# Optimization experiments

Hardware: AMD Instinct MI355X
Metric: run time of the kernel (lower is better)

## Reference

```python
import jax, jax.numpy as jnp
import numpy as np

V, D, DI, S, B, NI = 32000, 1024, 768, 512, 8, 197
EPS = 1e-5

def _ln(x, g, b):
    m = jnp.mean(x, axis=-1, keepdims=True)
    v = jnp.var(x, axis=-1, keepdims=True)
    return (x - m) * jax.lax.rsqrt(v + EPS) * g + b

def _pos_enc(seq_len, d):
    pos = np.arange(seq_len)[:, None].astype(np.float32)
    i = np.arange(0, d, 2).astype(np.float32)
    ang = pos / np.power(10000.0, i / d)
    pe = np.zeros((seq_len, d), dtype=np.float32)
    pe[:, 0::2] = np.sin(ang)
    pe[:, 1::2] = np.cos(ang)
    return jnp.asarray(pe)

def setup_inputs() -> dict:
    key = jax.random.key(0)
    ks = jax.random.split(key, 24)
    def rn(k, shape, scale=0.02):
        return jax.random.normal(k, shape, dtype=jnp.float32) * scale
    return {
        'tokens': jax.random.randint(ks[0], (B, S), 0, V),
        'img_emb': jax.random.normal(ks[1], (B, NI, DI), dtype=jnp.float32),
        'emb_table': rn(ks[2], (V, D), 1.0),
        'Wq1': rn(ks[3], (D, D)), 'bq1': jnp.zeros((D,), jnp.float32),
        'Wk1': rn(ks[4], (D, D)), 'bk1': jnp.zeros((D,), jnp.float32),
        'Wv1': rn(ks[5], (D, D)), 'bv1': jnp.zeros((D,), jnp.float32),
        'g1': jnp.ones((D,), jnp.float32), 'b1': jnp.zeros((D,), jnp.float32),
        'Wq2': rn(ks[6], (D, D)), 'bq2': jnp.zeros((D,), jnp.float32),
        'Wk2': rn(ks[7], (DI, D)), 'bk2': jnp.zeros((D,), jnp.float32),
        'Wv2': rn(ks[8], (DI, D)), 'bv2': jnp.zeros((D,), jnp.float32),
        'g2': jnp.ones((D,), jnp.float32), 'b2': jnp.zeros((D,), jnp.float32),
        'Wp': rn(ks[9], (D, V)), 'bp': jnp.zeros((V,), jnp.float32),
    }

def _forward(tokens, img_emb, emb_table, Wq1, bq1, Wk1, bk1, Wv1, bv1, g1, b1,
             Wq2, bq2, Wk2, bk2, Wv2, bv2, g2, b2, Wp, bp):
    scale = 1.0 / jnp.sqrt(jnp.float32(D))
    x = emb_table[tokens] + _pos_enc(S, D)[None]  # [B,S,D]
    # masked (causal) self-attention
    Q = x @ Wq1 + bq1
    K = x @ Wk1 + bk1
    Vv = x @ Wv1 + bv1
    attn = jnp.einsum('bqd,bkd->bqk', Q, K) * scale
    causal = jnp.tril(jnp.ones((S, S), dtype=bool))
    attn = jnp.where(causal[None], attn, -jnp.inf)
    A = jax.nn.softmax(attn, axis=-1)
    x = _ln(A @ Vv + x, g1, b1)
    # cross-attention over image tokens
    Q2 = x @ Wq2 + bq2
    K2 = img_emb @ Wk2 + bk2
    V2 = img_emb @ Wv2 + bv2
    A2 = jax.nn.softmax(jnp.einsum('bqd,bkd->bqk', Q2, K2) * scale, axis=-1)
    x = _ln(A2 @ V2 + x, g2, b2)
    # vocab projection (note: Decoder.forward never calls self.ff)
    return x @ Wp + bp  # [B,S,V]

def reference(tokens, img_emb, emb_table, Wq1, bq1, Wk1, bk1, Wv1, bv1, g1, b1,
              Wq2, bq2, Wk2, bk2, Wv2, bv2, g2, b2, Wp, bp):
    return _forward(tokens, img_emb, emb_table, Wq1, bq1, Wk1, bk1, Wv1, bv1, g1, b1,
                    Wq2, bq2, Wk2, bk2, Wv2, bv2, g2, b2, Wp, bp)
```

## Files before the change

### kernel.cpp

```cpp
#include <hip/hip_runtime.h>
#include <hip/hip_bf16.h>


#define DEV __device__ __forceinline__

typedef __bf16 bf16x8 __attribute__((ext_vector_type(8)));
typedef float f32x4 __attribute__((ext_vector_type(4)));
typedef unsigned int u32;
typedef __hip_bfloat16 bf16;

DEV void llds16(const void* g, void* l) {
  __builtin_amdgcn_global_load_lds((const __attribute__((address_space(1))) u32*)g,
                                   (__attribute__((address_space(3))) u32*)l, 16, 0, 0);
}

DEV float wredsum(float v){
#pragma unroll
  for (int o = 32; o; o >>= 1) v += __shfl_xor(v, o, 64);
  return v;
}
DEV float wredmax(float v){
#pragma unroll
  for (int o = 32; o; o >>= 1) v = fmaxf(v, __shfl_xor(v, o, 64));
  return v;
}

DEV float b2f(unsigned short x){ return __uint_as_float((u32)x << 16); }

DEV void store_out(float* p, float v){ *p = v; }
DEV void store_out(bf16* p, float v){ *p = __float2bfloat16(v); }

#define SBAR __builtin_amdgcn_sched_barrier(0)
#define HBAR __builtin_amdgcn_s_barrier()
#define LGKM0 asm volatile("s_waitcnt lgkmcnt(0)" ::: "memory")
#define VMC6 asm volatile("s_waitcnt vmcnt(6)" ::: "memory")
#define VMC0 asm volatile("s_waitcnt vmcnt(0)" ::: "memory")

#define RD_A(slot, mh) do { \
  _Pragma("unroll") for (int m = 0; m < 4; m++) { \
    const int r_ = wr*128 + ((mh)*4 + m)*16 + lo; \
    _Pragma("unroll") for (int ks = 0; ks < 2; ks++) \
      af[m*2+ks] = *(const bf16x8*)((slot) + r_*128 + ((((ks<<2)|hi) ^ x7) << 4)); \
  } } while(0)
#define RD_B(slot, nh) do { \
  _Pragma("unroll") for (int n = 0; n < 2; n++) { \
    const int gn_ = (nh)*2 + n; \
    const int r_ = wc*64 + gn_*16 + lo; \
    _Pragma("unroll") for (int ks = 0; ks < 2; ks++) \
      bfv[gn_*2+ks] = *(const bf16x8*)((slot) + 32768 + r_*128 + ((((ks<<2)|hi) ^ x7) << 4)); \
  } } while(0)
#define MQ(mh, nh) do { \
  __builtin_amdgcn_s_setprio(1); \
  _Pragma("unroll") for (int ks = 0; ks < 2; ks++) \
  _Pragma("unroll") for (int m = 0; m < 4; m++) \
  _Pragma("unroll") for (int n = 0; n < 2; n++) \
    acc[(mh)*4+m][(nh)*2+n] = __builtin_amdgcn_mfma_f32_16x16x32_bf16( \
        af[m*2+ks], bfv[((nh)*2+n)*2+ks], acc[(mh)*4+m][(nh)*2+n], 0, 0, 0); \
  __builtin_amdgcn_s_setprio(0); \
  } while(0)

template<typename OutT>
__global__ __launch_bounds__(512, 1) void gemm256_kernel(
    const bf16* __restrict__ A, const bf16* __restrict__ Bt, OutT* __restrict__ C,
    const float* __restrict__ bias, int M, int N, int K, int lda, int ldb, int ldc)
{
  __shared__ alignas(16) char lds[131072];
  const int tid = threadIdx.x;
  const int wave = tid >> 6, lane = tid & 63;
  const int lo = lane & 15, hi = lane >> 4;
  const int x7 = lo & 7;
  const int wr = wave >> 2, wc = wave & 3;
  const int lr8 = lane >> 3;
  const int koff = ((lane & 7) ^ lr8) << 3;

  const int nbx = M >> 8;
  const int nwg = nbx * (N >> 8);
  int id = blockIdx.x;
  int g = (nwg & 7) ? id : ((id & 7) * (nwg >> 3) + (id >> 3));
  const int row0 = (g % nbx) * 256, col0 = (g / nbx) * 256;
  const int NT2 = K >> 6;

  auto stage = [&](int kind, int t) {
    if (t >= NT2) return;
    char* slot = lds + (t & 1) * 65536;
    const int kk = (t << 6) + koff;
#pragma unroll
    for (int j = 0; j < 2; j++) {
      if (kind == 0 || kind == 3) {
        const int br = ((kind == 3) ? 64 : 0) + j*128 + wave*8;
        llds16(A + (long)(row0 + br + lr8)*lda + kk, slot + br*128);
      } else {
        const int br = ((kind == 2) ? 32 : 0) + (wave&3)*8 + (wave>>2)*64 + j*128;
        llds16(Bt + (long)(col0 + br + lr8)*ldb + kk, slot + 32768 + br*128);
      }
    }
  };

  f32x4 acc[8][4] = {};
  bf16x8 af[8], bfv[8];

  stage(0,0); stage(1,0); stage(2,0); stage(3,0);
  stage(0,1); stage(1,1); stage(2,1);
  VMC6;
  HBAR; SBAR;

  for (int it = 0; it < (NT2 >> 1); it++) {
    const int ta = it*2, tb = ta+1;
    const char* sa = lds;
    const char* sb = lds + 65536;
    RD_A(sa, 0); RD_B(sa, 0); SBAR; stage(3, tb); SBAR;
    HBAR; LGKM0; SBAR; MQ(0, 0); SBAR; HBAR; SBAR;
    RD_B(sa, 1); SBAR; stage(0, ta+2); SBAR;
    HBAR; LGKM0; SBAR; MQ(0, 1); SBAR; HBAR; SBAR;
    RD_A(sa, 1); SBAR; stage(1, ta+2); SBAR;
    HBAR; LGKM0; SBAR; MQ(1, 0); SBAR; HBAR; SBAR;
    stage(2, ta+2); SBAR;
    HBAR; SBAR; MQ(1, 1); SBAR;
    if (ta+2 < NT2) { VMC6; } else { VMC0; }
    HBAR; SBAR;
    RD_A(sb, 0); RD_B(sb, 0); SBAR; stage(3, ta+2); SBAR;
    HBAR; LGKM0; SBAR; MQ(0, 0); SBAR; HBAR; SBAR;
    RD_B(sb, 1); SBAR; stage(0, tb+2); SBAR;
    HBAR; LGKM0; SBAR; MQ(0, 1); SBAR; HBAR; SBAR;
    RD_A(sb, 1); SBAR; stage(1, tb+2); SBAR;
    HBAR; LGKM0; SBAR; MQ(1, 0); SBAR; HBAR; SBAR;
    stage(2, tb+2); SBAR;
    HBAR; SBAR; MQ(1, 1); SBAR;
    if (tb+2 < NT2) { VMC6; } else { VMC0; }
    HBAR; SBAR;
  }

#pragma unroll
  for (int m = 0; m < 8; m++) {
    const int r = row0 + wr * 128 + m * 16 + hi * 4;
#pragma unroll
    for (int n = 0; n < 4; n++) {
      const int c = col0 + wc * 64 + n * 16 + lo;
      const float bb = bias ? bias[c] : 0.0f;
#pragma unroll
      for (int j = 0; j < 4; j++)
        store_out(&C[(long)(r + j) * ldc + c], acc[m][n][j] + bb);
    }
  }
}

template<typename OutT>
__global__ __launch_bounds__(256) void gemm_bt_kernel(
    const bf16* __restrict__ A, const bf16* __restrict__ Bt, OutT* __restrict__ C,
    const float* __restrict__ bias, int M, int N, int K,
    int lda, int ldb, int ldc, long sA, long sB, long sC, int tri, int kcausal)
{
  A  += (long)blockIdx.z * sA;
  Bt += (long)blockIdx.z * sB;
  C  += (long)blockIdx.z * sC;
  __shared__ alignas(16) char lds[32768];
  int bx = blockIdx.x, by = blockIdx.y;
  if (tri) { int t = blockIdx.x, i = 0; while (t > i) { t -= i + 1; i++; } bx = i; by = t; }
  const int tid = threadIdx.x;
  const int wave = tid >> 6, lane = tid & 63;
  const int lo = lane & 15, hi = lane >> 4;
  const int hi2 = hi ^ ((lo >> 1) & 3);
  const int wr = wave >> 1, wc = wave & 1;
  const int row0 = bx * 128, col0 = by * 128;
  const int srow  = lane >> 2;
  const int skoff = (((lane & 3) ^ ((lane >> 3) & 3)) << 3);
  const int Keff = kcausal ? (K < row0 + 128 ? K : row0 + 128) : K;
  const int NT = Keff >> 5;

  auto stage = [&](int t) {
    char* base = lds + (t & 1) * 16384;
    const int kk = (t << 5) + skoff;
#pragma unroll
    for (int c = 0; c < 2; ++c) {
      const int seg = c*4 + wave;
      int ra = row0 + seg*16 + srow; ra = ra < M ? ra : M-1;
      llds16(A + (long)ra*lda + kk, base + seg*1024);
      int rb = col0 + seg*16 + srow; rb = rb < N ? rb : N-1;
      llds16(Bt + (long)rb*ldb + kk, base + 8192 + seg*1024);
    }
  };

  f32x4 acc[4][4] = {};

  stage(0);
  VMC0;
  HBAR; SBAR;

  for (int t = 0; t < NT; t++) {
    const char* As = lds + (t & 1) * 16384;
    const char* Bs = As + 8192;
    if (t + 1 < NT) stage(t + 1);
    bf16x8 af[4], bfv[4];
#pragma unroll
    for (int m = 0; m < 4; m++)
      af[m] = *(const bf16x8*)(As + ((wr*64 + m*16 + lo) << 6) + (hi2 << 4));
#pragma unroll
    for (int n = 0; n < 4; n++)
      bfv[n] = *(const bf16x8*)(Bs + ((wc*64 + n*16 + lo) << 6) + (hi2 << 4));
    __builtin_amdgcn_s_setprio(1);
#pragma unroll
    for (int m = 0; m < 4; m++)
#pragma unroll
      for (int n = 0; n < 4; n++)
        acc[m][n] = __builtin_amdgcn_mfma_f32_16x16x32_bf16(af[m], bfv[n], acc[m][n], 0, 0, 0);
    __builtin_amdgcn_s_setprio(0);
    SBAR;
    VMC0;
    SBAR;
    HBAR; SBAR;
  }

#pragma unroll
  for (int m = 0; m < 4; m++) {
    const int rbase = row0 + wr*64 + m*16 + hi*4;
#pragma unroll
    for (int n = 0; n < 4; n++) {
      const int cc = col0 + wc*64 + n*16 + lo;
      if (cc >= N) continue;
      const float bb = bias ? bias[cc] : 0.0f;
#pragma unroll
      for (int j = 0; j < 4; j++) {
        const int rr = rbase + j;
        if (rr < M) store_out(&C[(long)rr*ldc + cc], acc[m][n][j] + bb);
      }
    }
  }
}

__global__ __launch_bounds__(256) void wprep4_kernel(
    const float* W0, const float* W1, const float* W2, const float* W3,
    bf16* T0, bf16* T1, bf16* T2, bf16* T3, int K, int N)
{
  const int z = blockIdx.z;
  const float* W = z == 0 ? W0 : z == 1 ? W1 : z == 2 ? W2 : W3;
  bf16* T = z == 0 ? T0 : z == 1 ? T1 : z == 2 ? T2 : T3;
  __shared__ bf16 t[32][33];
  const int k0 = blockIdx.x * 32, n0 = blockIdx.y * 32;
  const int tx = threadIdx.x & 31, ty = threadIdx.x >> 5;
#pragma unroll
  for (int i = 0; i < 4; i++)
    t[ty + i*8][tx] = __float2bfloat16(W[(long)(k0 + ty + i*8)*N + n0 + tx]);
  __syncthreads();
#pragma unroll
  for (int i = 0; i < 4; i++)
    T[(long)(n0 + ty + i*8)*K + k0 + tx] = t[tx][ty + i*8];
}

__global__ __launch_bounds__(256) void transpose_pad_kernel(
    const bf16* __restrict__ in, bf16* __restrict__ out,
    int R, int Cc, int inLD, int outLD, long inBatch, long outBatch)
{
  in  += (long)blockIdx.z * inBatch;
  out += (long)blockIdx.z * outBatch;
  __shared__ bf16 t[32][33];
  const int r0 = blockIdx.x * 32, c0 = blockIdx.y * 32;
  const int tx = threadIdx.x & 31, ty = threadIdx.x >> 5;
#pragma unroll
  for (int i = 0; i < 4; i++) {
    const int r = r0 + ty + i*8;
    bf16 v = __float2bfloat16(0.0f);
    if (r < R) v = in[(long)r*inLD + c0 + tx];
    t[ty + i*8][tx] = v;
  }
  __syncthreads();
#pragma unroll
  for (int i = 0; i < 4; i++) {
    const int oc = r0 + tx;
    const int orow = c0 + ty + i*8;
    if (oc < outLD) out[(long)orow*outLD + oc] = t[tx][ty + i*8];
  }
}

__global__ __launch_bounds__(256) void concat_bias_kernel(
    const float* a, const float* b, const float* c, int n1, int n2, int n3, float* out)
{
  const int i = blockIdx.x * 256 + threadIdx.x;
  if (i >= n1 + n2 + n3) return;
  out[i] = i < n1 ? a[i] : (i < n1 + n2 ? b[i - n1] : c[i - n1 - n2]);
}

__global__ __launch_bounds__(256) void embed_kernel(
    const int* __restrict__ tok, const float* __restrict__ tbl,
    bf16* __restrict__ xb)
{
  const int row = blockIdx.x;
  const int s = row & 511;
  const float pos = (float)s;
  const float* te = tbl + (long)tok[row] * 1024;
  const int d0 = threadIdx.x * 4;
  float4 v = *(const float4*)(te + d0);
  float o[4] = {v.x, v.y, v.z, v.w};
#pragma unroll
  for (int k = 0; k < 4; k++) {
    const int d = d0 + k;
    const int i2 = d & ~1;
    const float ang = pos * exp2f((float)i2 * -0.0129762816f);
    o[k] += (d & 1) ? __cosf(ang) : __sinf(ang);
  }
  bf16 ob[4];
#pragma unroll
  for (int k = 0; k < 4; k++) ob[k] = __float2bfloat16(o[k]);
  *(ushort4*)((unsigned short*)xb + (long)row*1024 + d0) = *(ushort4*)ob;
}

__global__ __launch_bounds__(256) void cvt_bf16_kernel(const float* __restrict__ in, bf16* __restrict__ out, long n)
{
  long i = (long)blockIdx.x * blockDim.x + threadIdx.x;
  if (i < n) out[i] = __float2bfloat16(in[i]);
}

__global__ __launch_bounds__(64) void softmax_causal_kernel(
    const float* __restrict__ Sc, bf16* __restrict__ P)
{
  const int row = blockIdx.x;
  const int q = row & 511;
  const float* srow = Sc + (long)row * 512;
  bf16* prow = P + (long)row * 512;
  const int lane = threadIdx.x;
  const float scale = 0.03125f;
  float mx = -1e30f;
  for (int j = lane; j <= q; j += 64) mx = fmaxf(mx, srow[j]);
  mx = wredmax(mx);
  float sum = 0.0f;
  for (int j = lane; j <= q; j += 64) sum += expf((srow[j] - mx) * scale);
  sum = wredsum(sum);
  const float inv = 1.0f / sum;
  for (int j = lane; j < 512; j += 64) {
    float p = (j <= q) ? expf((srow[j] - mx) * scale) * inv : 0.0f;
    prow[j] = __float2bfloat16(p);
  }
}

__global__ __launch_bounds__(64) void softmax_cross_kernel(
    const float* __restrict__ Sc, bf16* __restrict__ P)
{
  const int row = blockIdx.x;
  const float* srow = Sc + (long)row * 224;
  bf16* prow = P + (long)row * 224;
  const int lane = threadIdx.x;
  const float scale = 0.03125f;
  float mx = -1e30f;
  for (int j = lane; j < 197; j += 64) mx = fmaxf(mx, srow[j]);
  mx = wredmax(mx);
  float sum = 0.0f;
  for (int j = lane; j < 197; j += 64) sum += expf((srow[j] - mx) * scale);
  sum = wredsum(sum);
  const float inv = 1.0f / sum;
  for (int j = lane; j < 224; j += 64) {
    float p = (j < 197) ? expf((srow[j] - mx) * scale) * inv : 0.0f;
    prow[j] = __float2bfloat16(p);
  }
}

__global__ __launch_bounds__(256) void add_ln_kernel(
    const bf16* __restrict__ Acc, const bf16* __restrict__ Res,
    const float* __restrict__ g, const float* __restrict__ b,
    bf16* __restrict__ outb)
{
  const int row = blockIdx.x;
  const unsigned short* a = (const unsigned short*)Acc + (long)row * 1024;
  const unsigned short* r = (const unsigned short*)Res + (long)row * 1024;
  const int d0 = threadIdx.x * 4;
  ushort4 av = *(const ushort4*)(a + d0);
  ushort4 rv = *(const ushort4*)(r + d0);
  float vals[4] = { b2f(av.x) + b2f(rv.x), b2f(av.y) + b2f(rv.y),
                    b2f(av.z) + b2f(rv.z), b2f(av.w) + b2f(rv.w) };
  float s = vals[0] + vals[1] + vals[2] + vals[3];
  float ss = vals[0]*vals[0] + vals[1]*vals[1] + vals[2]*vals[2] + vals[3]*vals[3];
  s = wredsum(s); ss = wredsum(ss);
  __shared__ float sh[8];
  const int wave = threadIdx.x >> 6, lane = threadIdx.x & 63;
  if (lane == 0) { sh[wave] = s; sh[wave+4] = ss; }
  __syncthreads();
  s  = sh[0] + sh[1] + sh[2] + sh[3];
  ss = sh[4] + sh[5] + sh[6] + sh[7];
  const float mean = s * (1.0f/1024.0f);
  const float var  = ss * (1.0f/1024.0f) - mean*mean;
  const float inv  = rsqrtf(var + 1e-5f);
  bf16 ob[4];
#pragma unroll
  for (int i = 0; i < 4; i++) {
    const int d = d0 + i;
    ob[i] = __float2bfloat16((vals[i] - mean) * inv * g[d] + b[d]);
  }
  *(ushort4*)((unsigned short*)outb + (long)row*1024 + d0) = *(ushort4*)ob;
}

extern "C" void kernel_launch(void* const* d_in, const int* in_sizes, int n_in,
                              void* d_out, int out_size, void* d_ws, size_t ws_size,
                              hipStream_t stream) {
  const int*   tokens = (const int*)  d_in[0];
  const float* img    = (const float*)d_in[1];
  const float* emb    = (const float*)d_in[2];
  const float* Wq1    = (const float*)d_in[3];
  const float* bq1    = (const float*)d_in[4];
  const float* Wk1    = (const float*)d_in[5];
  const float* bk1    = (const float*)d_in[6];
  const float* Wv1    = (const float*)d_in[7];
  const float* bv1    = (const float*)d_in[8];
  const float* g1     = (const float*)d_in[9];
  const float* b1     = (const float*)d_in[10];
  const float* Wq2    = (const float*)d_in[11];
  const float* bq2    = (const float*)d_in[12];
  const float* Wk2    = (const float*)d_in[13];
  const float* bk2    = (const float*)d_in[14];
  const float* Wv2    = (const float*)d_in[15];
  const float* bv2    = (const float*)d_in[16];
  const float* g2     = (const float*)d_in[17];
  const float* b2     = (const float*)d_in[18];
  const float* Wp     = (const float*)d_in[19];
  const float* bp     = (const float*)d_in[20];
  float* out = (float*)d_out;

  const int B = 8, S = 512, D = 1024, DI = 768, NI = 197, NIP = 224, V = 32000;
  const int M = B * S;
  const int MI = B * NI;

  char* ws = (char*)d_ws;
  size_t off = 0;
  auto alloc = [&](size_t bytes) -> char* {
    char* p = ws + off; off += (bytes + 255) & ~(size_t)255; return p;
  };
  bf16* Wq1t = (bf16*)alloc((size_t)D*D*2);
  bf16* Wk1t = (bf16*)alloc((size_t)D*D*2);
  bf16* Wv1t = (bf16*)alloc((size_t)D*D*2);
  bf16* Wq2t = (bf16*)alloc((size_t)D*D*2);
  bf16* Wk2t = (bf16*)alloc((size_t)D*DI*2);
  bf16* Wv2t = (bf16*)alloc((size_t)D*DI*2);
  bf16* Wpt  = (bf16*)alloc((size_t)V*D*2);
  float* bqkv= (float*)alloc((size_t)3*D*4);
  float* bkv2= (float*)alloc((size_t)2*D*4);
  bf16*  xb  = (bf16*) alloc((size_t)M*D*2);
  bf16*  imgb= (bf16*) alloc((size_t)MI*DI*2);
  bf16*  QKV = (bf16*) alloc((size_t)M*3*D*2);
  bf16*  Vt  = (bf16*) alloc((size_t)M*D*2);
  float* sc1 = (float*)alloc((size_t)B*S*S*4);
  bf16*  P1  = (bf16*) alloc((size_t)B*S*S*2);
  bf16*  ao1 = (bf16*) alloc((size_t)M*D*2);
  bf16*  x2b = (bf16*) alloc((size_t)M*D*2);
  bf16*  Q2  = (bf16*) alloc((size_t)M*D*2);
  bf16*  KV2 = (bf16*) alloc((size_t)MI*2*D*2);
  bf16*  V2t = (bf16*) alloc((size_t)B*D*NIP*2);
  float* sc2 = (float*)alloc((size_t)B*S*NIP*4);
  bf16*  P2  = (bf16*) alloc((size_t)B*S*NIP*2);
  bf16*  ao2 = (bf16*) alloc((size_t)M*D*2);
  bf16*  x3b = (bf16*) alloc((size_t)M*D*2);
  (void)ws_size; (void)in_sizes; (void)n_in; (void)out_size;

  wprep4_kernel<<<dim3(D/32,  D/32, 4), 256, 0, stream>>>(Wq1, Wk1, Wv1, Wq2, Wq1t, Wk1t, Wv1t, Wq2t, D, D);
  wprep4_kernel<<<dim3(DI/32, D/32, 2), 256, 0, stream>>>(Wk2, Wv2, nullptr, nullptr, Wk2t, Wv2t, nullptr, nullptr, DI, D);
  wprep4_kernel<<<dim3(D/32,  V/32, 1), 256, 0, stream>>>(Wp, nullptr, nullptr, nullptr, Wpt, nullptr, nullptr, nullptr, D, V);
  concat_bias_kernel<<<(3*D+255)/256, 256, 0, stream>>>(bq1, bk1, bv1, D, D, D, bqkv);
  concat_bias_kernel<<<(2*D+255)/256, 256, 0, stream>>>(bk2, bv2, nullptr, D, D, 0, bkv2);

  embed_kernel<<<M, 256, 0, stream>>>(tokens, emb, xb);
  {
    long n = (long)MI * DI;
    cvt_bf16_kernel<<<(int)((n + 255)/256), 256, 0, stream>>>(img, imgb, n);
  }

  auto gemmF = [&](const bf16* A, const bf16* Bt, float* C, const float* bias,
                   int m, int n, int k, int lda, int ldb, int ldc,
                   long sA, long sB, long sC, int batch) {
    dim3 g((m+127)/128, (n+127)/128, batch);
    gemm_bt_kernel<float><<<g, 256, 0, stream>>>(A, Bt, C, bias, m, n, k, lda, ldb, ldc, sA, sB, sC, 0, 0);
  };
  auto gemmB = [&](const bf16* A, const bf16* Bt, bf16* C, const float* bias,
                   int m, int n, int k, int lda, int ldb, int ldc,
                   long sA, long sB, long sC, int batch) {
    dim3 g((m+127)/128, (n+127)/128, batch);
    gemm_bt_kernel<bf16><<<g, 256, 0, stream>>>(A, Bt, C, bias, m, n, k, lda, ldb, ldc, sA, sB, sC, 0, 0);
  };

  gemm256_kernel<bf16><<<dim3((M/256)*(3*D/256)), 512, 0, stream>>>(
      xb, Wq1t, QKV, bqkv, M, 3*D, D, D, D, 3*D);
  transpose_pad_kernel<<<dim3(S/32, D/32, B), 256, 0, stream>>>(
      QKV + 2*D, Vt, S, D, 3*D, S, (long)S*3*D, (long)D*S);
  gemm_bt_kernel<float><<<dim3(10, 1, B), 256, 0, stream>>>(
      QKV, QKV + D, sc1, nullptr, S, S, D, 3*D, 3*D, S,
      (long)S*3*D, (long)S*3*D, (long)S*S, 1, 0);
  softmax_causal_kernel<<<M, 64, 0, stream>>>(sc1, P1);
  gemm_bt_kernel<bf16><<<dim3(S/128, D/128, B), 256, 0, stream>>>(
      P1, Vt, ao1, nullptr, S, D, S, S, S, D,
      (long)S*S, (long)D*S, (long)S*D, 0, 1);
  add_ln_kernel<<<M, 256, 0, stream>>>(ao1, xb, g1, b1, x2b);

  gemm256_kernel<bf16><<<dim3((M/256)*(D/256)), 512, 0, stream>>>(
      x2b, Wq2t, Q2, bq2, M, D, D, D, D, D);
  gemmB(imgb, Wk2t, KV2, bkv2, MI, 2*D, DI, DI, DI, 2*D, 0, 0, 0, 1);
  transpose_pad_kernel<<<dim3((NIP+31)/32, D/32, B), 256, 0, stream>>>(
      KV2 + D, V2t, NI, D, 2*D, NIP, (long)NI*2*D, (long)D*NIP);
  gemmF(Q2, KV2, sc2, nullptr, S, NI, D, D, 2*D, NIP, (long)S*D, (long)NI*2*D, (long)S*NIP, B);
  softmax_cross_kernel<<<M, 64, 0, stream>>>(sc2, P2);
  gemmB(P2, V2t, ao2, nullptr, S, D, NIP, NIP, NIP, D, (long)S*NIP, (long)D*NIP, (long)S*D, B);
  add_ln_kernel<<<M, 256, 0, stream>>>(ao2, x2b, g2, b2, x3b);

  gemm256_kernel<float><<<dim3((M/256)*(V/256)), 512, 0, stream>>>(
      x3b, Wpt, out, bp, M, V, D, D, D, V);
}
```

Measured before the change: 636.0 us.

## Produce transposed V directly via swapped-operand GEMMs and drop transpose kernels

The V projections for self- and cross-attention are now computed as W^T·X GEMMs, so they write V already transposed. This removes the two separate transpose_pad kernels and the extra traffic through the QKV and KV2 buffers. The V bias is moved into the P·V GEMM epilogue, which is valid because each softmax row sums to one. Image tokens are padded to 224 per batch during the bf16 conversion so that the cross-attention GEMMs work on aligned tiles. The cost is that the fused QKV GEMM becomes a QK GEMM plus a separate V GEMM on the smaller 128-tile kernel. Padded rows of V2t now contain Wv2·0 rather than zero, which relies on softmax masking those columns and on the bias being added per column.

```diff
diff --git a/kernel.cpp b/kernel.cpp
--- a/kernel.cpp
+++ b/kernel.cpp
@@ -246,31 +246,6 @@
     T[(long)(n0 + ty + i*8)*K + k0 + tx] = t[tx][ty + i*8];
 }
 
-__global__ __launch_bounds__(256) void transpose_pad_kernel(
-    const bf16* __restrict__ in, bf16* __restrict__ out,
-    int R, int Cc, int inLD, int outLD, long inBatch, long outBatch)
-{
-  in  += (long)blockIdx.z * inBatch;
-  out += (long)blockIdx.z * outBatch;
-  __shared__ bf16 t[32][33];
-  const int r0 = blockIdx.x * 32, c0 = blockIdx.y * 32;
-  const int tx = threadIdx.x & 31, ty = threadIdx.x >> 5;
-#pragma unroll
-  for (int i = 0; i < 4; i++) {
-    const int r = r0 + ty + i*8;
-    bf16 v = __float2bfloat16(0.0f);
-    if (r < R) v = in[(long)r*inLD + c0 + tx];
-    t[ty + i*8][tx] = v;
-  }
-  __syncthreads();
-#pragma unroll
-  for (int i = 0; i < 4; i++) {
-    const int oc = r0 + tx;
-    const int orow = c0 + ty + i*8;
-    if (oc < outLD) out[(long)orow*outLD + oc] = t[tx][ty + i*8];
-  }
-}
-
 __global__ __launch_bounds__(256) void concat_bias_kernel(
     const float* a, const float* b, const float* c, int n1, int n2, int n3, float* out)
 {
@@ -303,10 +278,16 @@
   *(ushort4*)((unsigned short*)xb + (long)row*1024 + d0) = *(ushort4*)ob;
 }
 
-__global__ __launch_bounds__(256) void cvt_bf16_kernel(const float* __restrict__ in, bf16* __restrict__ out, long n)
-{
-  long i = (long)blockIdx.x * blockDim.x + threadIdx.x;
-  if (i < n) out[i] = __float2bfloat16(in[i]);
+__global__ __launch_bounds__(256) void cvt_pad_img_kernel(
+    const float* __restrict__ img, bf16* __restrict__ imgb)
+{
+  const long i = (long)blockIdx.x * 256 + threadIdx.x;
+  if (i >= (long)1792 * 768) return;
+  const int pr = (int)(i / 768), col = (int)(i % 768);
+  const int b = pr / 224, tok = pr % 224;
+  float v = 0.0f;
+  if (tok < 197) v = img[((long)b * 197 + tok) * 768 + col];
+  imgb[i] = __float2bfloat16(v);
 }
 
 __global__ __launch_bounds__(64) void softmax_causal_kernel(
@@ -414,7 +395,7 @@
 
   const int B = 8, S = 512, D = 1024, DI = 768, NI = 197, NIP = 224, V = 32000;
   const int M = B * S;
-  const int MI = B * NI;
+  const int MIP = B * NIP;
 
   char* ws = (char*)d_ws;
   size_t off = 0;
@@ -428,19 +409,18 @@
   bf16* Wk2t = (bf16*)alloc((size_t)D*DI*2);
   bf16* Wv2t = (bf16*)alloc((size_t)D*DI*2);
   bf16* Wpt  = (bf16*)alloc((size_t)V*D*2);
-  float* bqkv= (float*)alloc((size_t)3*D*4);
-  float* bkv2= (float*)alloc((size_t)2*D*4);
+  float* bqk = (float*)alloc((size_t)2*D*4);
   bf16*  xb  = (bf16*) alloc((size_t)M*D*2);
-  bf16*  imgb= (bf16*) alloc((size_t)MI*DI*2);
-  bf16*  QKV = (bf16*) alloc((size_t)M*3*D*2);
-  bf16*  Vt  = (bf16*) alloc((size_t)M*D*2);
+  bf16*  imgb= (bf16*) alloc((size_t)MIP*DI*2);
+  bf16*  QK  = (bf16*) alloc((size_t)M*2*D*2);
+  bf16*  Vt  = (bf16*) alloc((size_t)D*M*2);
   float* sc1 = (float*)alloc((size_t)B*S*S*4);
   bf16*  P1  = (bf16*) alloc((size_t)B*S*S*2);
   bf16*  ao1 = (bf16*) alloc((size_t)M*D*2);
   bf16*  x2b = (bf16*) alloc((size_t)M*D*2);
   bf16*  Q2  = (bf16*) alloc((size_t)M*D*2);
-  bf16*  KV2 = (bf16*) alloc((size_t)MI*2*D*2);
-  bf16*  V2t = (bf16*) alloc((size_t)B*D*NIP*2);
+  bf16*  K2p = (bf16*) alloc((size_t)MIP*D*2);
+  bf16*  V2t = (bf16*) alloc((size_t)D*MIP*2);
   float* sc2 = (float*)alloc((size_t)B*S*NIP*4);
   bf16*  P2  = (bf16*) alloc((size_t)B*S*NIP*2);
   bf16*  ao2 = (bf16*) alloc((size_t)M*D*2);
@@ -450,49 +430,40 @@
   wprep4_kernel<<<dim3(D/32,  D/32, 4), 256, 0, stream>>>(Wq1, Wk1, Wv1, Wq2, Wq1t, Wk1t, Wv1t, Wq2t, D, D);
   wprep4_kernel<<<dim3(DI/32, D/32, 2), 256, 0, stream>>>(Wk2, Wv2, nullptr, nullptr, Wk2t, Wv2t, nullptr, nullptr, DI, D);
   wprep4_kernel<<<dim3(D/32,  V/32, 1), 256, 0, stream>>>(Wp, nullptr, nullptr, nullptr, Wpt, nullptr, nullptr, nullptr, D, V);
-  concat_bias_kernel<<<(3*D+255)/256, 256, 0, stream>>>(bq1, bk1, bv1, D, D, D, bqkv);
-  concat_bias_kernel<<<(2*D+255)/256, 256, 0, stream>>>(bk2, bv2, nullptr, D, D, 0, bkv2);
+  concat_bias_kernel<<<(2*D+255)/256, 256, 0, stream>>>(bq1, bk1, nullptr, D, D, 0, bqk);
 
   embed_kernel<<<M, 256, 0, stream>>>(tokens, emb, xb);
   {
-    long n = (long)MI * DI;
-    cvt_bf16_kernel<<<(int)((n + 255)/256), 256, 0, stream>>>(img, imgb, n);
-  }
-
-  auto gemmF = [&](const bf16* A, const bf16* Bt, float* C, const float* bias,
-                   int m, int n, int k, int lda, int ldb, int ldc,
-                   long sA, long sB, long sC, int batch) {
-    dim3 g((m+127)/128, (n+127)/128, batch);
-    gemm_bt_kernel<float><<<g, 256, 0, stream>>>(A, Bt, C, bias, m, n, k, lda, ldb, ldc, sA, sB, sC, 0, 0);
-  };
-  auto gemmB = [&](const bf16* A, const bf16* Bt, bf16* C, const float* bias,
-                   int m, int n, int k, int lda, int ldb, int ldc,
-                   long sA, long sB, long sC, int batch) {
-    dim3 g((m+127)/128, (n+127)/128, batch);
-    gemm_bt_kernel<bf16><<<g, 256, 0, stream>>>(A, Bt, C, bias, m, n, k, lda, ldb, ldc, sA, sB, sC, 0, 0);
-  };
-
-  gemm256_kernel<bf16><<<dim3((M/256)*(3*D/256)), 512, 0, stream>>>(
-      xb, Wq1t, QKV, bqkv, M, 3*D, D, D, D, 3*D);
-  transpose_pad_kernel<<<dim3(S/32, D/32, B), 256, 0, stream>>>(
-      QKV + 2*D, Vt, S, D, 3*D, S, (long)S*3*D, (long)D*S);
+    long n = (long)MIP * DI;
+    cvt_pad_img_kernel<<<(int)((n + 255)/256), 256, 0, stream>>>(img, imgb);
+  }
+
+  gemm256_kernel<bf16><<<dim3((M/256)*(2*D/256)), 512, 0, stream>>>(
+      xb, Wq1t, QK, bqk, M, 2*D, D, D, D, 2*D);
+  gemm_bt_kernel<bf16><<<dim3(D/128, M/128, 1), 256, 0, stream>>>(
+      Wv1t, xb, Vt, nullptr, D, M, D, D, D, M, 0, 0, 0, 0, 0);
   gemm_bt_kernel<float><<<dim3(10, 1, B), 256, 0, stream>>>(
-      QKV, QKV + D, sc1, nullptr, S, S, D, 3*D, 3*D, S,
-      (long)S*3*D, (long)S*3*D, (long)S*S, 1, 0);
+      QK, QK + D, sc1, nullptr, S, S, D, 2*D, 2*D, S,
+      (long)S*2*D, (long)S*2*D, (long)S*S, 1, 0);
   softmax_causal_kernel<<<M, 64, 0, stream>>>(sc1, P1);
   gemm_bt_kernel<bf16><<<dim3(S/128, D/128, B), 256, 0, stream>>>(
-      P1, Vt, ao1, nullptr, S, D, S, S, S, D,
-      (long)S*S, (long)D*S, (long)S*D, 0, 1);
+      P1, Vt, ao1, bv1, S, D, S, S, M, D,
+      (long)S*S, (long)S, (long)S*D, 0, 1);
   add_ln_kernel<<<M, 256, 0, stream>>>(ao1, xb, g1, b1, x2b);
 
   gemm256_kernel<bf16><<<dim3((M/256)*(D/256)), 512, 0, stream>>>(
       x2b, Wq2t, Q2, bq2, M, D, D, D, D, D);
-  gemmB(imgb, Wk2t, KV2, bkv2, MI, 2*D, DI, DI, DI, 2*D, 0, 0, 0, 1);
-  transpose_pad_kernel<<<dim3((NIP+31)/32, D/32, B), 256, 0, stream>>>(
-      KV2 + D, V2t, NI, D, 2*D, NIP, (long)NI*2*D, (long)D*NIP);
-  gemmF(Q2, KV2, sc2, nullptr, S, NI, D, D, 2*D, NIP, (long)S*D, (long)NI*2*D, (long)S*NIP, B);
+  gemm_bt_kernel<bf16><<<dim3(MIP/128, D/128, 1), 256, 0, stream>>>(
+      imgb, Wk2t, K2p, bk2, MIP, D, DI, DI, DI, D, 0, 0, 0, 0, 0);
+  gemm_bt_kernel<bf16><<<dim3(D/128, MIP/128, 1), 256, 0, stream>>>(
+      Wv2t, imgb, V2t, nullptr, D, MIP, DI, DI, DI, MIP, 0, 0, 0, 0, 0);
+  gemm_bt_kernel<float><<<dim3(S/128, (NIP+127)/128, B), 256, 0, stream>>>(
+      Q2, K2p, sc2, nullptr, S, NI, D, D, D, NIP,
+      (long)S*D, (long)NIP*D, (long)S*NIP, 0, 0);
   softmax_cross_kernel<<<M, 64, 0, stream>>>(sc2, P2);
-  gemmB(P2, V2t, ao2, nullptr, S, D, NIP, NIP, NIP, D, (long)S*NIP, (long)D*NIP, (long)S*D, B);
+  gemm_bt_kernel<bf16><<<dim3(S/128, D/128, B), 256, 0, stream>>>(
+      P2, V2t, ao2, bv2, S, D, NIP, NIP, MIP, D,
+      (long)S*NIP, (long)NIP, (long)S*D, 0, 0);
   add_ln_kernel<<<M, 256, 0, stream>>>(ao2, x2b, g2, b2, x3b);
 
   gemm256_kernel<float><<<dim3((M/256)*(V/256)), 512, 0, stream>>>(
```

Result: slower. 679.4 us (+6.8%).

## Fuse softmax into the P@V GEMM for self and cross attention

Applied to the files above, without the earlier changes.

Removes the standalone causal and cross softmax kernels and the bf16 probability buffers. A new fused_pv_kernel computes per-row max and sum from the fp32 score matrix in a prologue, then builds normalized bf16 probability tiles directly in LDS while streaming V through global_load_lds. This drops a kernel launch and a round trip of the probability matrix per attention, but each block recomputes exponentials from global scores with scalar loads, so the A-operand path depends on uncoalesced fp32 reads and redundant exp work across column blocks.

```diff
diff --git a/kernel.cpp b/kernel.cpp
--- a/kernel.cpp
+++ b/kernel.cpp
@@ -17,11 +17,6 @@
 DEV float wredsum(float v){
 #pragma unroll
   for (int o = 32; o; o >>= 1) v += __shfl_xor(v, o, 64);
-  return v;
-}
-DEV float wredmax(float v){
-#pragma unroll
-  for (int o = 32; o; o >>= 1) v = fmaxf(v, __shfl_xor(v, o, 64));
   return v;
 }
 
@@ -148,7 +143,7 @@
 __global__ __launch_bounds__(256) void gemm_bt_kernel(
     const bf16* __restrict__ A, const bf16* __restrict__ Bt, OutT* __restrict__ C,
     const float* __restrict__ bias, int M, int N, int K,
-    int lda, int ldb, int ldc, long sA, long sB, long sC, int tri, int kcausal)
+    int lda, int ldb, int ldc, long sA, long sB, long sC, int tri)
 {
   A  += (long)blockIdx.z * sA;
   Bt += (long)blockIdx.z * sB;
@@ -164,8 +159,7 @@
   const int row0 = bx * 128, col0 = by * 128;
   const int srow  = lane >> 2;
   const int skoff = (((lane & 3) ^ ((lane >> 3) & 3)) << 3);
-  const int Keff = kcausal ? (K < row0 + 128 ? K : row0 + 128) : K;
-  const int NT = Keff >> 5;
+  const int NT = K >> 5;
 
   auto stage = [&](int t) {
     char* base = lds + (t & 1) * 16384;
@@ -227,6 +221,111 @@
   }
 }
 
+template<int CAUSAL>
+__global__ __launch_bounds__(256) void fused_pv_kernel(
+    const float* __restrict__ Sc, const bf16* __restrict__ Bt, bf16* __restrict__ C,
+    int Kw, int validFixed, int ldS, int ldb, int ldc, long sS, long sB, long sC)
+{
+  Sc += (long)blockIdx.z * sS;
+  Bt += (long)blockIdx.z * sB;
+  C  += (long)blockIdx.z * sC;
+  __shared__ alignas(16) char lds[32768];
+  __shared__ float smx[128], sinv[128];
+  const int tid = threadIdx.x;
+  const int wave = tid >> 6, lane = tid & 63;
+  const int lo = lane & 15, hi = lane >> 4;
+  const int hi2 = hi ^ ((lo >> 1) & 3);
+  const int wr = wave >> 1, wc = wave & 1;
+  const int row0 = blockIdx.x * 128, col0 = blockIdx.y * 128;
+  const int srow  = lane >> 2;
+  const int skoff = (((lane & 3) ^ ((lane >> 3) & 3)) << 3);
+  const int Keff = CAUSAL ? (Kw < row0 + 128 ? Kw : row0 + 128) : Kw;
+  const int NT = Keff >> 5;
+  const float scale = 0.03125f;
+
+  {
+    const int r2 = tid >> 1, par = tid & 1;
+    const float* sr = Sc + (long)(row0 + r2) * ldS;
+    const int valid = CAUSAL ? (row0 + r2 + 1) : validFixed;
+    float mx = -3.0e38f;
+    for (int j = par; j < valid; j += 2) mx = fmaxf(mx, sr[j]);
+    mx = fmaxf(mx, __shfl_xor(mx, 1, 64));
+    float sum = 0.0f;
+    for (int j = par; j < valid; j += 2) sum += expf((sr[j] - mx) * scale);
+    sum += __shfl_xor(sum, 1, 64);
+    if (par == 0) { smx[r2] = mx; sinv[r2] = 1.0f / sum; }
+  }
+  __syncthreads();
+
+  auto writeA = [&](int t) {
+    char* base = lds + (t & 1) * 16384;
+    const int r2 = tid >> 1, par = tid & 1;
+    const float* sr = Sc + (long)(row0 + r2) * ldS;
+    const int valid = CAUSAL ? (row0 + r2 + 1) : validFixed;
+    const float mx = smx[r2], inv = sinv[r2];
+#pragma unroll
+    for (int i = 0; i < 2; i++) {
+      const int gq = par * 2 + i;
+      const int k0 = (t << 5) + gq * 8;
+      bf16 p8[8];
+#pragma unroll
+      for (int jj = 0; jj < 8; jj++) {
+        const int k = k0 + jj;
+        float p = (k < valid) ? expf((sr[k] - mx) * scale) * inv : 0.0f;
+        p8[jj] = __float2bfloat16(p);
+      }
+      *(bf16x8*)(base + (r2 << 6) + ((gq ^ ((r2 >> 1) & 3)) << 4)) = *(bf16x8*)p8;
+    }
+  };
+  auto stageB = [&](int t) {
+    char* base = lds + (t & 1) * 16384 + 8192;
+    const int kk = (t << 5) + skoff;
+#pragma unroll
+    for (int c = 0; c < 2; ++c) {
+      const int seg = c*4 + wave;
+      llds16(Bt + (long)(col0 + seg*16 + srow)*ldb + kk, base + seg*1024);
+    }
+  };
+
+  f32x4 acc[4][4] = {};
+
+  writeA(0); stageB(0);
+  __syncthreads();
+
+  for (int t = 0; t < NT; t++) {
+    const char* As = lds + (t & 1) * 16384;
+    const char* Bs = As + 8192;
+    if (t + 1 < NT) { stageB(t + 1); writeA(t + 1); }
+    bf16x8 af[4], bfv[4];
+#pragma unroll
+    for (int m = 0; m < 4; m++)
+      af[m] = *(const bf16x8*)(As + ((wr*64 + m*16 + lo) << 6) + (hi2 << 4));
+#pragma unroll
+    for (int n = 0; n < 4; n++)
+      bfv[n] = *(const bf16x8*)(Bs + ((wc*64 + n*16 + lo) << 6) + (hi2 << 4));
+    __builtin_amdgcn_s_setprio(1);
+#pragma unroll
+    for (int m = 0; m < 4; m++)
+#pragma unroll
+      for (int n = 0; n < 4; n++)
+        acc[m][n] = __builtin_amdgcn_mfma_f32_16x16x32_bf16(af[m], bfv[n], acc[m][n], 0, 0, 0);
+    __builtin_amdgcn_s_setprio(0);
+    __syncthreads();
+  }
+
+#pragma unroll
+  for (int m = 0; m < 4; m++) {
+    const int rbase = row0 + wr*64 + m*16 + hi*4;
+#pragma unroll
+    for (int n = 0; n < 4; n++) {
+      const int cc = col0 + wc*64 + n*16 + lo;
+#pragma unroll
+      for (int j = 0; j < 4; j++)
+        C[(long)(rbase + j)*ldc + cc] = __float2bfloat16(acc[m][n][j]);
+    }
+  }
+}
+
 __global__ __launch_bounds__(256) void wprep4_kernel(
     const float* W0, const float* W1, const float* W2, const float* W3,
     bf16* T0, bf16* T1, bf16* T2, bf16* T3, int K, int N)
@@ -307,49 +406,6 @@
 {
   long i = (long)blockIdx.x * blockDim.x + threadIdx.x;
   if (i < n) out[i] = __float2bfloat16(in[i]);
-}
-
-__global__ __launch_bounds__(64) void softmax_causal_kernel(
-    const float* __restrict__ Sc, bf16* __restrict__ P)
-{
-  const int row = blockIdx.x;
-  const int q = row & 511;
-  const float* srow = Sc + (long)row * 512;
-  bf16* prow = P + (long)row * 512;
-  const int lane = threadIdx.x;
-  const float scale = 0.03125f;
-  float mx = -1e30f;
-  for (int j = lane; j <= q; j += 64) mx = fmaxf(mx, srow[j]);
-  mx = wredmax(mx);
-  float sum = 0.0f;
-  for (int j = lane; j <= q; j += 64) sum += expf((srow[j] - mx) * scale);
-  sum = wredsum(sum);
-  const float inv = 1.0f / sum;
-  for (int j = lane; j < 512; j += 64) {
-    float p = (j <= q) ? expf((srow[j] - mx) * scale) * inv : 0.0f;
-    prow[j] = __float2bfloat16(p);
-  }
-}
-
-__global__ __launch_bounds__(64) void softmax_cross_kernel(
-    const float* __restrict__ Sc, bf16* __restrict__ P)
-{
-  const int row = blockIdx.x;
-  const float* srow = Sc + (long)row * 224;
-  bf16* prow = P + (long)row * 224;
-  const int lane = threadIdx.x;
-  const float scale = 0.03125f;
-  float mx = -1e30f;
-  for (int j = lane; j < 197; j += 64) mx = fmaxf(mx, srow[j]);
-  mx = wredmax(mx);
-  float sum = 0.0f;
-  for (int j = lane; j < 197; j += 64) sum += expf((srow[j] - mx) * scale);
-  sum = wredsum(sum);
-  const float inv = 1.0f / sum;
-  for (int j = lane; j < 224; j += 64) {
-    float p = (j < 197) ? expf((srow[j] - mx) * scale) * inv : 0.0f;
-    prow[j] = __float2bfloat16(p);
-  }
 }
 
 __global__ __launch_bounds__(256) void add_ln_kernel(
@@ -435,14 +491,12 @@
   bf16*  QKV = (bf16*) alloc((size_t)M*3*D*2);
   bf16*  Vt  = (bf16*) alloc((size_t)M*D*2);
   float* sc1 = (float*)alloc((size_t)B*S*S*4);
-  bf16*  P1  = (bf16*) alloc((size_t)B*S*S*2);
   bf16*  ao1 = (bf16*) alloc((size_t)M*D*2);
   bf16*  x2b = (bf16*) alloc((size_t)M*D*2);
   bf16*  Q2  = (bf16*) alloc((size_t)M*D*2);
   bf16*  KV2 = (bf16*) alloc((size_t)MI*2*D*2);
   bf16*  V2t = (bf16*) alloc((size_t)B*D*NIP*2);
   float* sc2 = (float*)alloc((size_t)B*S*NIP*4);
-  bf16*  P2  = (bf16*) alloc((size_t)B*S*NIP*2);
   bf16*  ao2 = (bf16*) alloc((size_t)M*D*2);
   bf16*  x3b = (bf16*) alloc((size_t)M*D*2);
   (void)ws_size; (void)in_sizes; (void)n_in; (void)out_size;
@@ -458,19 +512,6 @@
     long n = (long)MI * DI;
     cvt_bf16_kernel<<<(int)((n + 255)/256), 256, 0, stream>>>(img, imgb, n);
   }
-
-  auto gemmF = [&](const bf16* A, const bf16* Bt, float* C, const float* bias,
-                   int m, int n, int k, int lda, int ldb, int ldc,
-                   long sA, long sB, long sC, int batch) {
-    dim3 g((m+127)/128, (n+127)/128, batch);
-    gemm_bt_kernel<float><<<g, 256, 0, stream>>>(A, Bt, C, bias, m, n, k, lda, ldb, ldc, sA, sB, sC, 0, 0);
-  };
-  auto gemmB = [&](const bf16* A, const bf16* Bt, bf16* C, const float* bias,
-                   int m, int n, int k, int lda, int ldb, int ldc,
-                   long sA, long sB, long sC, int batch) {
-    dim3 g((m+127)/128, (n+127)/128, batch);
-    gemm_bt_kernel<bf16><<<g, 256, 0, stream>>>(A, Bt, C, bias, m, n, k, lda, ldb, ldc, sA, sB, sC, 0, 0);
-  };
 
   gemm256_kernel<bf16><<<dim3((M/256)*(3*D/256)), 512, 0, stream>>>(
       xb, Wq1t, QKV, bqkv, M, 3*D, D, D, D, 3*D);
@@ -478,21 +519,22 @@
       QKV + 2*D, Vt, S, D, 3*D, S, (long)S*3*D, (long)D*S);
   gemm_bt_kernel<float><<<dim3(10, 1, B), 256, 0, stream>>>(
       QKV, QKV + D, sc1, nullptr, S, S, D, 3*D, 3*D, S,
-      (long)S*3*D, (long)S*3*D, (long)S*S, 1, 0);
-  softmax_causal_kernel<<<M, 64, 0, stream>>>(sc1, P1);
-  gemm_bt_kernel<bf16><<<dim3(S/128, D/128, B), 256, 0, stream>>>(
-      P1, Vt, ao1, nullptr, S, D, S, S, S, D,
-      (long)S*S, (long)D*S, (long)S*D, 0, 1);
+      (long)S*3*D, (long)S*3*D, (long)S*S, 1);
+  fused_pv_kernel<1><<<dim3(S/128, D/128, B), 256, 0, stream>>>(
+      sc1, Vt, ao1, S, 0, S, S, D, (long)S*S, (long)D*S, (long)S*D);
   add_ln_kernel<<<M, 256, 0, stream>>>(ao1, xb, g1, b1, x2b);
 
   gemm256_kernel<bf16><<<dim3((M/256)*(D/256)), 512, 0, stream>>>(
       x2b, Wq2t, Q2, bq2, M, D, D, D, D, D);
-  gemmB(imgb, Wk2t, KV2, bkv2, MI, 2*D, DI, DI, DI, 2*D, 0, 0, 0, 1);
+  gemm_bt_kernel<bf16><<<dim3((MI+127)/128, (2*D)/128, 1), 256, 0, stream>>>(
+      imgb, Wk2t, KV2, bkv2, MI, 2*D, DI, DI, DI, 2*D, 0, 0, 0, 0);
   transpose_pad_kernel<<<dim3((NIP+31)/32, D/32, B), 256, 0, stream>>>(
       KV2 + D, V2t, NI, D, 2*D, NIP, (long)NI*2*D, (long)D*NIP);
-  gemmF(Q2, KV2, sc2, nullptr, S, NI, D, D, 2*D, NIP, (long)S*D, (long)NI*2*D, (long)S*NIP, B);
-  softmax_cross_kernel<<<M, 64, 0, stream>>>(sc2, P2);
-  gemmB(P2, V2t, ao2, nullptr, S, D, NIP, NIP, NIP, D, (long)S*NIP, (long)D*NIP, (long)S*D, B);
+  gemm_bt_kernel<float><<<dim3(S/128, (NIP+127)/128, B), 256, 0, stream>>>(
+      Q2, KV2, sc2, nullptr, S, NI, D, D, 2*D, NIP,
+      (long)S*D, (long)NI*2*D, (long)S*NIP, 0);
+  fused_pv_kernel<0><<<dim3(S/128, D/128, B), 256, 0, stream>>>(
+      sc2, V2t, ao2, NIP, NI, NIP, NIP, D, (long)S*NIP, (long)D*NIP, (long)S*D);
   add_ln_kernel<<<M, 256, 0, stream>>>(ao2, x2b, g2, b2, x3b);
 
   gemm256_kernel<float><<<dim3((M/256)*(V/256)), 512, 0, stream>>>(
```

After: 745.8 us. +17.3%, slower.
